# Kernel tuning notes

Measured on AMD Instinct MI355X. Metric: run time of the kernel, lower is better.

## Reference

```python
import math
import jax, jax.numpy as jnp
import numpy as np

B, Q, K, D = 16, 2048, 2048, 128

def setup_inputs() -> dict:
    key = jax.random.key(0)
    kq, kk, kv, kl = jax.random.split(key, 4)
    queries = jax.random.normal(kq, (B, Q, D), dtype=jnp.float32)
    keys = jax.random.normal(kk, (B, K, D), dtype=jnp.float32)
    values = jax.random.normal(kv, (B, K, D), dtype=jnp.float32)
    valid_lens = jax.random.randint(kl, (B,), 0, K, dtype=jnp.int64)
    return {"queries": queries, "keys": keys, "values": values, "valid_lens": valid_lens}

def reference(queries, keys, values, valid_lens):
    d = queries.shape[-1]
    # [B, Q, K] scores
    scores = jnp.einsum("bqd,bkd->bqk", queries, keys) / math.sqrt(d)
    # Original masks X[index][length:] = -1e6, i.e. along the QUERY axis (dim 1),
    # filling entire rows; softmax over the key axis then yields uniform weights
    # for those rows. Reproduce exactly.
    q_idx = jnp.arange(queries.shape[1])  # [Q]
    mask = q_idx[None, :, None] >= valid_lens[:, None, None]  # [B, Q, 1]
    scores = jnp.where(mask, jnp.float32(-1000000.0), scores)
    attention_weights = jax.nn.softmax(scores, axis=-1)
    # dropout p=0.0 (eval) -> identity
    return jnp.einsum("bqk,bkd->bqd", attention_weights, values)
```

## Files before the change

### kernel.cpp

```cpp
#include <hip/hip_runtime.h>
#include <hip/hip_bf16.h>
#include <math.h>


#define Bn 16
#define Qn 2048
#define Kn 2048
#define Dn 128
#define SCALE 0.08838834764831845f

typedef _Float16 f16;
typedef _Float16 f16x8_t __attribute__((ext_vector_type(8)));
typedef float f32x16_t __attribute__((ext_vector_type(16)));

typedef __attribute__((address_space(1))) const unsigned int glb_u32;
typedef __attribute__((address_space(3))) unsigned int lds_u32;

__device__ __forceinline__ void g2l16(const void* g, void* l) {
  __builtin_amdgcn_global_load_lds((glb_u32*)g, (lds_u32*)l, 16, 0, 0);
}


__global__ void __launch_bounds__(256) prep_kernel(
    const float* __restrict__ Kg, const float* __restrict__ Vg,
    f16* __restrict__ Kh, f16* __restrict__ Vt, float* __restrict__ sv) {
  __shared__ float ps[8][32];
  const int b = blockIdx.z;
  const int x = threadIdx.x, y = threadIdx.y;

  {
    const int lb = (b * 4 + blockIdx.y) * 32 + blockIdx.x;
    const int t = y * 32 + x;
    const size_t key = (size_t)lb * 16 + (t >> 4);
    const int G = t & 15;
    const float* kp = Kg + (key << 7) + G * 8;
    float4 f0 = *(const float4*)kp;
    float4 f1 = *(const float4*)(kp + 4);
    f16x8_t o;
    o[0] = (f16)f0.x; o[1] = (f16)f0.y; o[2] = (f16)f0.z; o[3] = (f16)f0.w;
    o[4] = (f16)f1.x; o[5] = (f16)f1.y; o[6] = (f16)f1.z; o[7] = (f16)f1.w;
    const int gs = (G & 8) | ((G & 7) ^ ((int)key & 7));
    *(f16x8_t*)(Kh + (key << 7) + (gs << 3)) = o;
  }

  const int k0 = blockIdx.x * 64, d0 = blockIdx.y * 32;
  const int d = d0 + x;
  const float* vp = Vg + ((size_t)b * Kn + k0 + y * 8) * Dn + d;
  float s = 0.f;
  f16x8_t gr;
#pragma unroll
  for (int j = 0; j < 8; j++) {
    float v = vp[(size_t)j * Dn];
    s += v;
    gr[j] = (f16)v;
  }
  {
    const int kb = k0 >> 6;
    const int G = y;
    const int gs = G ^ (d & 7);
    *(f16x8_t*)(Vt + (((size_t)(b * (Kn / 64) + kb) * 128 + d) << 6) + (gs << 3)) = gr;
  }

  ps[y][x] = s;
  __syncthreads();
  if (y == 0) {
    float tot = 0.f;
#pragma unroll
    for (int j = 0; j < 8; j++) tot += ps[j][x];
    atomicAdd(&sv[b * Dn + d0 + x], tot);
  }
}

__device__ __forceinline__ int load_vl(const int* __restrict__ vlp, int b) {
  bool is64 = true;
#pragma unroll
  for (int i = 1; i < 16; i += 2) is64 = is64 && (vlp[i] == 0);
  return is64 ? vlp[2 * b] : vlp[b];
}


template <int S>
__global__ void __launch_bounds__(256, 2) flash_kernel(
    const float* __restrict__ Qg, const f16* __restrict__ Kh,
    const f16* __restrict__ Vt, const int* __restrict__ vlp,
    f16* __restrict__ Po, float* __restrict__ Lb) {
  const int b = blockIdx.y;
  const int seg = blockIdx.z;
  const int qt = (blockIdx.x * 5 + seg * 3) & 15;
  const int q0 = qt * 128;
  const int vl = load_vl(vlp, b);
  if (q0 >= vl) return;

  __shared__ __align__(16) f16 Ks[64 * 128];
  __shared__ __align__(16) f16 Vs[128 * 64];

  const int tid = threadIdx.x;
  const int wave = tid >> 6, lane = tid & 63;
  const int H = lane >> 5, l5 = lane & 31;
  const int qbase = q0 + wave * 32;
  const bool act = qbase < vl;
  const int q_lane = qbase + l5;
  const float sc = (q_lane >= vl) ? 0.f : SCALE;

  const int krow = (l5 & 0x13) | ((l5 & 4) << 1) | ((l5 & 8) >> 1);
  const int krow7 = krow & 7;

  f16x8_t qf[8];
  if (act) {
    const float* qp = Qg + ((size_t)b * Qn + q_lane) * Dn + 8 * H;
#pragma unroll
    for (int s = 0; s < 8; s++) {
      float4 f0 = *(const float4*)(qp + 16 * s);
      float4 f1 = *(const float4*)(qp + 16 * s + 4);
      f16x8_t q8;
      q8[0] = (f16)f0.x; q8[1] = (f16)f0.y; q8[2] = (f16)f0.z; q8[3] = (f16)f0.w;
      q8[4] = (f16)f1.x; q8[5] = (f16)f1.y; q8[6] = (f16)f1.z; q8[7] = (f16)f1.w;
      qf[s] = q8;
    }
  }

  f32x16_t O[4];
#pragma unroll
  for (int i = 0; i < 4; i++) O[i] = (f32x16_t)(0.f);
  float l_lane = 0.f;

  const char* KgT = (const char*)Kh + (((size_t)b * Kn + (size_t)seg * (Kn / S)) << 8);
  const char* VgT = (const char*)Vt + ((size_t)(b * (Kn / 64) + seg * (Kn / S) / 64) << 14);

  for (int it = 0; it < (Kn / S) / 64; it++) {
    __syncthreads();
    const char* kg = KgT + (size_t)it * 16384 + wave * 4096 + lane * 16;
    const char* vg = VgT + (size_t)it * 16384 + wave * 4096 + lane * 16;
    f16* kl = Ks + wave * 2048;
    f16* vli = Vs + wave * 2048;
#pragma unroll
    for (int i = 0; i < 4; i++) {
      g2l16(kg + i * 1024, kl + i * 512);
      g2l16(vg + i * 1024, vli + i * 512);
    }
    __syncthreads();

    if (act) {
#pragma unroll
      for (int sub = 0; sub < 2; sub++) {
        f32x16_t T = (f32x16_t)(0.f);
        const f16* krp = Ks + ((sub * 32 + krow) << 7);
#pragma unroll
        for (int s = 0; s < 8; s++) {
          const int G = 2 * s + H;
          const int gs = (G & 8) | ((G & 7) ^ krow7);
          f16x8_t kf = *(const f16x8_t*)(krp + (gs << 3));
          T = __builtin_amdgcn_mfma_f32_32x32x16_f16(kf, qf[s], T, 0, 0, 0);
        }

        f16x8_t pf0, pf1;
        float ls = 0.f;
#pragma unroll
        for (int r = 0; r < 8; r++) {
          float p = __expf(T[r] * sc);
          ls += p;
          pf0[r] = (f16)p;
        }
#pragma unroll
        for (int r = 8; r < 16; r++) {
          float p = __expf(T[r] * sc);
          ls += p;
          pf1[r - 8] = (f16)p;
        }
        l_lane += ls;

#pragma unroll
        for (int dt = 0; dt < 4; dt++) {
          const f16* vrp = Vs + ((dt * 32 + l5) << 6);
          const int G0 = sub * 4 + H, G1 = sub * 4 + 2 + H;
          const int gs0 = G0 ^ (l5 & 7);
          const int gs1 = G1 ^ (l5 & 7);
          f16x8_t vf0 = *(const f16x8_t*)(vrp + (gs0 << 3));
          f16x8_t vf1 = *(const f16x8_t*)(vrp + (gs1 << 3));
          O[dt] = __builtin_amdgcn_mfma_f32_32x32x16_f16(pf0, vf0, O[dt], 0, 0, 0);
          O[dt] = __builtin_amdgcn_mfma_f32_32x32x16_f16(pf1, vf1, O[dt], 0, 0, 0);
        }
      }
    }
  }

  if (!act) return;

  l_lane += __shfl_xor(l_lane, 32);
  if (lane < 32) Lb[(size_t)(seg * Bn + b) * Qn + qbase + l5] = l_lane;

  f16* po = Po + ((size_t)(seg * Bn + b) * Qn + qbase) * Dn;
#pragma unroll
  for (int dt = 0; dt < 4; dt++) {
#pragma unroll
    for (int r = 0; r < 16; r++) {
      const int qrow = (r & 3) + 8 * (r >> 2) + 4 * H;
      po[(size_t)qrow * Dn + dt * 32 + l5] = (f16)O[dt][r];
    }
  }
}


template <int S>
__global__ void __launch_bounds__(256) combine_kernel(
    const f16* __restrict__ Po, const float* __restrict__ Lb,
    const float* __restrict__ sv, const int* __restrict__ vlp,
    float* __restrict__ Out) {
  const int b = blockIdx.y, q0 = blockIdx.x * 64;
  const int vl = load_vl(vlp, b);
  const int tid = threadIdx.x;

  __shared__ float linv[64];
  if (tid < 64) {
    float s = 0.f;
#pragma unroll
    for (int sg = 0; sg < S; sg++) s += Lb[(size_t)(sg * Bn + b) * Qn + q0 + tid];
    linv[tid] = 1.0f / s;
  }
  __syncthreads();

  const int row16 = tid >> 4;
  const int d8 = (tid & 15) * 8;
  const float invK = 1.0f / (float)Kn;
  float mv[8];
#pragma unroll
  for (int j = 0; j < 8; j++) mv[j] = sv[b * Dn + d8 + j] * invK;

#pragma unroll
  for (int pass = 0; pass < 4; pass++) {
    const int row = pass * 16 + row16;
    const int q = q0 + row;
    float acc[8];
    if (q >= vl) {
#pragma unroll
      for (int j = 0; j < 8; j++) acc[j] = mv[j];
    } else {
#pragma unroll
      for (int j = 0; j < 8; j++) acc[j] = 0.f;
#pragma unroll
      for (int sg = 0; sg < S; sg++) {
        f16x8_t v = *(const f16x8_t*)(Po + ((size_t)(sg * Bn + b) * Qn + q) * Dn + d8);
#pragma unroll
        for (int j = 0; j < 8; j++) acc[j] += (float)v[j];
      }
      const float li = linv[row];
#pragma unroll
      for (int j = 0; j < 8; j++) acc[j] *= li;
    }
    float4 o0 = make_float4(acc[0], acc[1], acc[2], acc[3]);
    float4 o1 = make_float4(acc[4], acc[5], acc[6], acc[7]);
    float* op = Out + ((size_t)b * Qn + q) * Dn + d8;
    *(float4*)op = o0;
    *(float4*)(op + 4) = o1;
  }
}


extern "C" void kernel_launch(void* const* d_in, const int* in_sizes, int n_in,
                              void* d_out, int out_size, void* d_ws, size_t ws_size,
                              hipStream_t stream) {
  const float* Qg = (const float*)d_in[0];
  const float* Kg = (const float*)d_in[1];
  const float* Vg = (const float*)d_in[2];
  const int* vl = (const int*)d_in[3];
  float* Out = (float*)d_out;

  char* ws = (char*)d_ws;
  float* sumV = (float*)ws;
  f16* Kh = (f16*)(ws + 8192);
  f16* Vt = (f16*)(ws + 8192 + (size_t)Bn * Kn * Dn * 2);
  const size_t base = 8192 + 2 * (size_t)Bn * Kn * Dn * 2;
  f16* Po = (f16*)(ws + base);

  const size_t po8 = (size_t)8 * Bn * Qn * Dn * 2;
  const size_t lb8 = (size_t)8 * Bn * Qn * 4;
  const size_t po4 = (size_t)4 * Bn * Qn * Dn * 2;
  const size_t need8 = base + po8 + lb8;

  hipMemsetAsync(sumV, 0, Bn * Dn * sizeof(float), stream);
  prep_kernel<<<dim3(32, 4, Bn), dim3(32, 8), 0, stream>>>(Kg, Vg, Kh, Vt, sumV);

  if (ws_size >= need8) {
    float* Lb = (float*)(ws + base + po8);
    flash_kernel<8><<<dim3(16, Bn, 8), 256, 0, stream>>>(Qg, Kh, Vt, vl, Po, Lb);
    combine_kernel<8><<<dim3(Qn / 64, Bn), 256, 0, stream>>>(Po, Lb, sumV, vl, Out);
  } else {
    float* Lb = (float*)(ws + base + po4);
    flash_kernel<4><<<dim3(16, Bn, 4), 256, 0, stream>>>(Qg, Kh, Vt, vl, Po, Lb);
    combine_kernel<4><<<dim3(Qn / 64, Bn), 256, 0, stream>>>(Po, Lb, sumV, vl, Out);
  }
}
```

Before: 152.7 us.

## Add KV-stationary flash kernel splitting keys into 16 segments with fp16 Q

Adds a new flash kernel that keeps a 128-key K/V tile resident in LDS and loops over query tiles, splitting the key axis into 16 segments that are merged by a 16-way combine. The prep kernel now also converts Q to fp16 and lays V out in 128-key blocks, so the flash kernel loads Q fragments directly without fp32 conversion. The aim is to load each K/V tile once per block instead of once per query tile. In exchange it needs a larger workspace for 16 partial-output planes and writes and reads more partial data in the combine step. The older sequence-split path stays as a fallback when the workspace is too small.

```diff
diff --git a/kernel.cpp b/kernel.cpp
--- a/kernel.cpp
+++ b/kernel.cpp
@@ -21,9 +21,11 @@
 }
 
 
+template <int VT>
 __global__ void __launch_bounds__(256) prep_kernel(
-    const float* __restrict__ Kg, const float* __restrict__ Vg,
-    f16* __restrict__ Kh, f16* __restrict__ Vt, float* __restrict__ sv) {
+    const float* __restrict__ Qg, const float* __restrict__ Kg,
+    const float* __restrict__ Vg, f16* __restrict__ Qh, f16* __restrict__ Kh,
+    f16* __restrict__ Vt, float* __restrict__ sv) {
   __shared__ float ps[8][32];
   const int b = blockIdx.z;
   const int x = threadIdx.x, y = threadIdx.y;
@@ -41,6 +43,15 @@
     o[4] = (f16)f1.x; o[5] = (f16)f1.y; o[6] = (f16)f1.z; o[7] = (f16)f1.w;
     const int gs = (G & 8) | ((G & 7) ^ ((int)key & 7));
     *(f16x8_t*)(Kh + (key << 7) + (gs << 3)) = o;
+    if (Qh != nullptr) {
+      const float* qp = Qg + (key << 7) + G * 8;
+      float4 q0 = *(const float4*)qp;
+      float4 q1 = *(const float4*)(qp + 4);
+      f16x8_t oq;
+      oq[0] = (f16)q0.x; oq[1] = (f16)q0.y; oq[2] = (f16)q0.z; oq[3] = (f16)q0.w;
+      oq[4] = (f16)q1.x; oq[5] = (f16)q1.y; oq[6] = (f16)q1.z; oq[7] = (f16)q1.w;
+      *(f16x8_t*)(Qh + (key << 7) + G * 8) = oq;
+    }
   }
 
   const int k0 = blockIdx.x * 64, d0 = blockIdx.y * 32;
@@ -54,7 +65,12 @@
     s += v;
     gr[j] = (f16)v;
   }
-  {
+  if (VT == 128) {
+    const int kb = k0 >> 7;
+    const int G = ((k0 & 64) >> 3) + y;
+    const int gs = (G & 8) | ((G & 7) ^ (d & 7));
+    *(f16x8_t*)(Vt + (((size_t)(b * (Kn / 128) + kb) * 128 + d) << 7) + (gs << 3)) = gr;
+  } else {
     const int kb = k0 >> 6;
     const int G = y;
     const int gs = G ^ (d & 7);
@@ -79,8 +95,121 @@
 }
 
 
+template <int J>
+__global__ void __launch_bounds__(256, 2) flash_q(
+    const f16* __restrict__ Qh, const f16* __restrict__ Kh,
+    const f16* __restrict__ Vt, const int* __restrict__ vlp,
+    f16* __restrict__ Po, float* __restrict__ Lb) {
+  const int b = blockIdx.y;
+  const int seg = blockIdx.x & 15;
+  const int j = blockIdx.x >> 4;
+  const int vl = load_vl(vlp, b);
+  const int nq = (vl + 127) >> 7;
+  if (nq == 0) return;
+
+  __shared__ __align__(16) f16 Ks[128 * 128];
+  __shared__ __align__(16) f16 Vs[128 * 128];
+
+  const int tid = threadIdx.x;
+  const int wave = tid >> 6, lane = tid & 63;
+  const int H = lane >> 5, l5 = lane & 31;
+
+  {
+    const char* kg = (const char*)Kh + (((size_t)b * Kn + seg * 128) << 8) +
+                     wave * 8192 + lane * 16;
+    const char* vg = (const char*)Vt + ((size_t)(b * (Kn / 128) + seg) << 15) +
+                     wave * 8192 + lane * 16;
+    f16* kl = Ks + wave * 4096;
+    f16* vli = Vs + wave * 4096;
+#pragma unroll
+    for (int i = 0; i < 8; i++) {
+      g2l16(kg + i * 1024, kl + i * 512);
+      g2l16(vg + i * 1024, vli + i * 512);
+    }
+  }
+  __syncthreads();
+
+  const int krow = (l5 & 0x13) | ((l5 & 4) << 1) | ((l5 & 8) >> 1);
+  const int krow7 = krow & 7;
+
+  for (int qt = j; qt < nq; qt += J) {
+    const int q0 = qt << 7;
+    const int qbase = q0 + wave * 32;
+    if (qbase >= vl) continue;
+    const int q_lane = qbase + l5;
+    const float sc = (q_lane >= vl) ? 0.f : SCALE;
+
+    f16x8_t qf[8];
+    {
+      const f16* qp = Qh + ((size_t)b * Qn + q_lane) * Dn + 8 * H;
+#pragma unroll
+      for (int s = 0; s < 8; s++) qf[s] = *(const f16x8_t*)(qp + 16 * s);
+    }
+
+    f32x16_t O[4];
+#pragma unroll
+    for (int i = 0; i < 4; i++) O[i] = (f32x16_t)(0.f);
+    float l_lane = 0.f;
+
+#pragma unroll
+    for (int sub = 0; sub < 4; sub++) {
+      f32x16_t T = (f32x16_t)(0.f);
+      const f16* krp = Ks + ((sub * 32 + krow) << 7);
+#pragma unroll
+      for (int s = 0; s < 8; s++) {
+        const int G = 2 * s + H;
+        const int gs = (G & 8) | ((G & 7) ^ krow7);
+        f16x8_t kf = *(const f16x8_t*)(krp + (gs << 3));
+        T = __builtin_amdgcn_mfma_f32_32x32x16_f16(kf, qf[s], T, 0, 0, 0);
+      }
+
+      f16x8_t pf0, pf1;
+      float ls = 0.f;
+#pragma unroll
+      for (int r = 0; r < 8; r++) {
+        float p = __expf(T[r] * sc);
+        ls += p;
+        pf0[r] = (f16)p;
+      }
+#pragma unroll
+      for (int r = 8; r < 16; r++) {
+        float p = __expf(T[r] * sc);
+        ls += p;
+        pf1[r - 8] = (f16)p;
+      }
+      l_lane += ls;
+
+#pragma unroll
+      for (int dt = 0; dt < 4; dt++) {
+        const f16* vrp = Vs + ((dt * 32 + l5) << 7);
+        const int G0 = sub * 4 + H, G1 = sub * 4 + 2 + H;
+        const int gs0 = (G0 & 8) | ((G0 & 7) ^ (l5 & 7));
+        const int gs1 = (G1 & 8) | ((G1 & 7) ^ (l5 & 7));
+        f16x8_t vf0 = *(const f16x8_t*)(vrp + (gs0 << 3));
+        f16x8_t vf1 = *(const f16x8_t*)(vrp + (gs1 << 3));
+        O[dt] = __builtin_amdgcn_mfma_f32_32x32x16_f16(pf0, vf0, O[dt], 0, 0, 0);
+        O[dt] = __builtin_amdgcn_mfma_f32_32x32x16_f16(pf1, vf1, O[dt], 0, 0, 0);
+      }
+    }
+
+    float ll = l_lane + __shfl_xor(l_lane, 32);
+    if (lane < 32) Lb[(size_t)(seg * Bn + b) * Qn + qbase + l5] = ll;
+
+    f16* po = Po + ((size_t)(seg * Bn + b) * Qn + qbase) * Dn;
+#pragma unroll
+    for (int dt = 0; dt < 4; dt++) {
+#pragma unroll
+      for (int r = 0; r < 16; r++) {
+        const int qrow = (r & 3) + 8 * (r >> 2) + 4 * H;
+        po[(size_t)qrow * Dn + dt * 32 + l5] = (f16)O[dt][r];
+      }
+    }
+  }
+}
+
+
 template <int S>
-__global__ void __launch_bounds__(256, 2) flash_kernel(
+__global__ void __launch_bounds__(256, 2) flash_seq(
     const float* __restrict__ Qg, const f16* __restrict__ Kh,
     const f16* __restrict__ Vt, const int* __restrict__ vlp,
     f16* __restrict__ Po, float* __restrict__ Lb) {
@@ -152,7 +281,6 @@
           f16x8_t kf = *(const f16x8_t*)(krp + (gs << 3));
           T = __builtin_amdgcn_mfma_f32_32x32x16_f16(kf, qf[s], T, 0, 0, 0);
         }
-
         f16x8_t pf0, pf1;
         float ls = 0.f;
 #pragma unroll
@@ -168,7 +296,6 @@
           pf1[r - 8] = (f16)p;
         }
         l_lane += ls;
-
 #pragma unroll
         for (int dt = 0; dt < 4; dt++) {
           const f16* vrp = Vs + ((dt * 32 + l5) << 6);
@@ -266,27 +393,40 @@
   float* Out = (float*)d_out;
 
   char* ws = (char*)d_ws;
+  const size_t kv = (size_t)Bn * Kn * Dn * 2;
   float* sumV = (float*)ws;
   f16* Kh = (f16*)(ws + 8192);
-  f16* Vt = (f16*)(ws + 8192 + (size_t)Bn * Kn * Dn * 2);
-  const size_t base = 8192 + 2 * (size_t)Bn * Kn * Dn * 2;
-  f16* Po = (f16*)(ws + base);
-
-  const size_t po8 = (size_t)8 * Bn * Qn * Dn * 2;
-  const size_t lb8 = (size_t)8 * Bn * Qn * 4;
-  const size_t po4 = (size_t)4 * Bn * Qn * Dn * 2;
-  const size_t need8 = base + po8 + lb8;
+  f16* Vt = (f16*)(ws + 8192 + kv);
+
+  const size_t plane = (size_t)Bn * Qn * Dn * 2;
+  const size_t lplane = (size_t)Bn * Qn * 4;
+  const size_t need16 = 8192 + 3 * kv + 16 * plane + 16 * lplane;
+  const size_t base8 = 8192 + 2 * kv;
+  const size_t need8 = base8 + 8 * plane + 8 * lplane;
 
   hipMemsetAsync(sumV, 0, Bn * Dn * sizeof(float), stream);
-  prep_kernel<<<dim3(32, 4, Bn), dim3(32, 8), 0, stream>>>(Kg, Vg, Kh, Vt, sumV);
-
-  if (ws_size >= need8) {
-    float* Lb = (float*)(ws + base + po8);
-    flash_kernel<8><<<dim3(16, Bn, 8), 256, 0, stream>>>(Qg, Kh, Vt, vl, Po, Lb);
+
+  if (ws_size >= need16) {
+    f16* Qh = (f16*)(ws + 8192 + 2 * kv);
+    f16* Po = (f16*)(ws + 8192 + 3 * kv);
+    float* Lb = (float*)(ws + 8192 + 3 * kv + 16 * plane);
+    prep_kernel<128><<<dim3(32, 4, Bn), dim3(32, 8), 0, stream>>>(
+        Qg, Kg, Vg, Qh, Kh, Vt, sumV);
+    flash_q<2><<<dim3(32, Bn), 256, 0, stream>>>(Qh, Kh, Vt, vl, Po, Lb);
+    combine_kernel<16><<<dim3(Qn / 64, Bn), 256, 0, stream>>>(Po, Lb, sumV, vl, Out);
+  } else if (ws_size >= need8) {
+    f16* Po = (f16*)(ws + base8);
+    float* Lb = (float*)(ws + base8 + 8 * plane);
+    prep_kernel<64><<<dim3(32, 4, Bn), dim3(32, 8), 0, stream>>>(
+        Qg, Kg, Vg, (f16*)nullptr, Kh, Vt, sumV);
+    flash_seq<8><<<dim3(16, Bn, 8), 256, 0, stream>>>(Qg, Kh, Vt, vl, Po, Lb);
     combine_kernel<8><<<dim3(Qn / 64, Bn), 256, 0, stream>>>(Po, Lb, sumV, vl, Out);
   } else {
-    float* Lb = (float*)(ws + base + po4);
-    flash_kernel<4><<<dim3(16, Bn, 4), 256, 0, stream>>>(Qg, Kh, Vt, vl, Po, Lb);
+    f16* Po = (f16*)(ws + base8);
+    float* Lb = (float*)(ws + base8 + 4 * plane);
+    prep_kernel<64><<<dim3(32, 4, Bn), dim3(32, 8), 0, stream>>>(
+        Qg, Kg, Vg, (f16*)nullptr, Kh, Vt, sumV);
+    flash_seq<4><<<dim3(16, Bn, 4), 256, 0, stream>>>(Qg, Kh, Vt, vl, Po, Lb);
     combine_kernel<4><<<dim3(Qn / 64, Bn), 256, 0, stream>>>(Po, Lb, sumV, vl, Out);
   }
 }
```

After: 144.3 us. -5.5%, faster.

## Fuse K/V conversion into flash kernel with key-segment-resident LDS tiles

Applied to the files above, without the earlier changes.

Removes the separate prep kernel and has each flash block load and convert a 128-key segment of K and V (with a transposed V) straight into LDS, where it stays for every query tile that block handles. The grid becomes 16 key segments times 2 query-tile groups per batch, and the combine step now reduces 16 partial outputs. This saves the f16 staging round trip through global memory and one launch, but every block reloads fp32 K/V, V is read with strided column loads, and the partial-output buffer and combine traffic grow.

```diff
diff --git a/kernel.cpp b/kernel.cpp
--- a/kernel.cpp
+++ b/kernel.cpp
@@ -13,64 +13,6 @@
 typedef _Float16 f16x8_t __attribute__((ext_vector_type(8)));
 typedef float f32x16_t __attribute__((ext_vector_type(16)));
 
-typedef __attribute__((address_space(1))) const unsigned int glb_u32;
-typedef __attribute__((address_space(3))) unsigned int lds_u32;
-
-__device__ __forceinline__ void g2l16(const void* g, void* l) {
-  __builtin_amdgcn_global_load_lds((glb_u32*)g, (lds_u32*)l, 16, 0, 0);
-}
-
-
-__global__ void __launch_bounds__(256) prep_kernel(
-    const float* __restrict__ Kg, const float* __restrict__ Vg,
-    f16* __restrict__ Kh, f16* __restrict__ Vt, float* __restrict__ sv) {
-  __shared__ float ps[8][32];
-  const int b = blockIdx.z;
-  const int x = threadIdx.x, y = threadIdx.y;
-
-  {
-    const int lb = (b * 4 + blockIdx.y) * 32 + blockIdx.x;
-    const int t = y * 32 + x;
-    const size_t key = (size_t)lb * 16 + (t >> 4);
-    const int G = t & 15;
-    const float* kp = Kg + (key << 7) + G * 8;
-    float4 f0 = *(const float4*)kp;
-    float4 f1 = *(const float4*)(kp + 4);
-    f16x8_t o;
-    o[0] = (f16)f0.x; o[1] = (f16)f0.y; o[2] = (f16)f0.z; o[3] = (f16)f0.w;
-    o[4] = (f16)f1.x; o[5] = (f16)f1.y; o[6] = (f16)f1.z; o[7] = (f16)f1.w;
-    const int gs = (G & 8) | ((G & 7) ^ ((int)key & 7));
-    *(f16x8_t*)(Kh + (key << 7) + (gs << 3)) = o;
-  }
-
-  const int k0 = blockIdx.x * 64, d0 = blockIdx.y * 32;
-  const int d = d0 + x;
-  const float* vp = Vg + ((size_t)b * Kn + k0 + y * 8) * Dn + d;
-  float s = 0.f;
-  f16x8_t gr;
-#pragma unroll
-  for (int j = 0; j < 8; j++) {
-    float v = vp[(size_t)j * Dn];
-    s += v;
-    gr[j] = (f16)v;
-  }
-  {
-    const int kb = k0 >> 6;
-    const int G = y;
-    const int gs = G ^ (d & 7);
-    *(f16x8_t*)(Vt + (((size_t)(b * (Kn / 64) + kb) * 128 + d) << 6) + (gs << 3)) = gr;
-  }
-
-  ps[y][x] = s;
-  __syncthreads();
-  if (y == 0) {
-    float tot = 0.f;
-#pragma unroll
-    for (int j = 0; j < 8; j++) tot += ps[j][x];
-    atomicAdd(&sv[b * Dn + d0 + x], tot);
-  }
-}
-
 __device__ __forceinline__ int load_vl(const int* __restrict__ vlp, int b) {
   bool is64 = true;
 #pragma unroll
@@ -79,123 +21,150 @@
 }
 
 
-template <int S>
-__global__ void __launch_bounds__(256, 2) flash_kernel(
-    const float* __restrict__ Qg, const f16* __restrict__ Kh,
-    const f16* __restrict__ Vt, const int* __restrict__ vlp,
-    f16* __restrict__ Po, float* __restrict__ Lb) {
+template <int J>
+__global__ void __launch_bounds__(256, 2) flash_g(
+    const float* __restrict__ Qg, const float* __restrict__ Kg,
+    const float* __restrict__ Vg, const int* __restrict__ vlp,
+    f16* __restrict__ Po, float* __restrict__ Lb, float* __restrict__ sv) {
   const int b = blockIdx.y;
-  const int seg = blockIdx.z;
-  const int qt = (blockIdx.x * 5 + seg * 3) & 15;
-  const int q0 = qt * 128;
+  const int seg = blockIdx.x & 15;
+  const int j = blockIdx.x >> 4;
   const int vl = load_vl(vlp, b);
-  if (q0 >= vl) return;
-
-  __shared__ __align__(16) f16 Ks[64 * 128];
-  __shared__ __align__(16) f16 Vs[128 * 64];
+  const int nq = (vl + 127) >> 7;
+  const int k0 = seg * 128;
+
+  __shared__ __align__(16) f16 Ks[128 * 128];
+  __shared__ __align__(16) f16 Vs[128 * 128];
 
   const int tid = threadIdx.x;
+
+  {
+    const int kk = tid >> 1, half = tid & 1;
+    const float* kp = Kg + ((size_t)b * Kn + k0 + kk) * Dn + half * 64;
+    f16* krow_p = Ks + kk * 128;
+    const int kk7 = kk & 7;
+#pragma unroll
+    for (int i = 0; i < 8; i++) {
+      const int G = half * 8 + i;
+      float4 f0 = *(const float4*)(kp + i * 8);
+      float4 f1 = *(const float4*)(kp + i * 8 + 4);
+      f16x8_t o;
+      o[0] = (f16)f0.x; o[1] = (f16)f0.y; o[2] = (f16)f0.z; o[3] = (f16)f0.w;
+      o[4] = (f16)f1.x; o[5] = (f16)f1.y; o[6] = (f16)f1.z; o[7] = (f16)f1.w;
+      const int gs = (G & 8) | ((G & 7) ^ kk7);
+      *(f16x8_t*)(krow_p + gs * 8) = o;
+    }
+  }
+
+  {
+    const int d = tid >> 1, half = tid & 1;
+    const float* vp = Vg + ((size_t)b * Kn + k0 + half * 64) * Dn + d;
+    f16* vrow_p = Vs + d * 128;
+    const int d7 = d & 7;
+    float colsum = 0.f;
+#pragma unroll
+    for (int i = 0; i < 8; i++) {
+      const int G = half * 8 + i;
+      f16x8_t o;
+#pragma unroll
+      for (int e = 0; e < 8; e++) {
+        float v = vp[(size_t)(i * 8 + e) * Dn];
+        o[e] = (f16)v;
+        colsum += v;
+      }
+      const int gs = (G & 8) | ((G & 7) ^ d7);
+      *(f16x8_t*)(vrow_p + gs * 8) = o;
+    }
+    if (j == 0) atomicAdd(&sv[b * Dn + d], colsum);
+  }
+  __syncthreads();
+
+  if (nq == 0) return;
+
   const int wave = tid >> 6, lane = tid & 63;
   const int H = lane >> 5, l5 = lane & 31;
-  const int qbase = q0 + wave * 32;
-  const bool act = qbase < vl;
-  const int q_lane = qbase + l5;
-  const float sc = (q_lane >= vl) ? 0.f : SCALE;
 
   const int krow = (l5 & 0x13) | ((l5 & 4) << 1) | ((l5 & 8) >> 1);
   const int krow7 = krow & 7;
 
-  f16x8_t qf[8];
-  if (act) {
-    const float* qp = Qg + ((size_t)b * Qn + q_lane) * Dn + 8 * H;
-#pragma unroll
-    for (int s = 0; s < 8; s++) {
-      float4 f0 = *(const float4*)(qp + 16 * s);
-      float4 f1 = *(const float4*)(qp + 16 * s + 4);
-      f16x8_t q8;
-      q8[0] = (f16)f0.x; q8[1] = (f16)f0.y; q8[2] = (f16)f0.z; q8[3] = (f16)f0.w;
-      q8[4] = (f16)f1.x; q8[5] = (f16)f1.y; q8[6] = (f16)f1.z; q8[7] = (f16)f1.w;
-      qf[s] = q8;
-    }
-  }
-
-  f32x16_t O[4];
-#pragma unroll
-  for (int i = 0; i < 4; i++) O[i] = (f32x16_t)(0.f);
-  float l_lane = 0.f;
-
-  const char* KgT = (const char*)Kh + (((size_t)b * Kn + (size_t)seg * (Kn / S)) << 8);
-  const char* VgT = (const char*)Vt + ((size_t)(b * (Kn / 64) + seg * (Kn / S) / 64) << 14);
-
-  for (int it = 0; it < (Kn / S) / 64; it++) {
-    __syncthreads();
-    const char* kg = KgT + (size_t)it * 16384 + wave * 4096 + lane * 16;
-    const char* vg = VgT + (size_t)it * 16384 + wave * 4096 + lane * 16;
-    f16* kl = Ks + wave * 2048;
-    f16* vli = Vs + wave * 2048;
-#pragma unroll
-    for (int i = 0; i < 4; i++) {
-      g2l16(kg + i * 1024, kl + i * 512);
-      g2l16(vg + i * 1024, vli + i * 512);
-    }
-    __syncthreads();
-
-    if (act) {
-#pragma unroll
-      for (int sub = 0; sub < 2; sub++) {
-        f32x16_t T = (f32x16_t)(0.f);
-        const f16* krp = Ks + ((sub * 32 + krow) << 7);
-#pragma unroll
-        for (int s = 0; s < 8; s++) {
-          const int G = 2 * s + H;
-          const int gs = (G & 8) | ((G & 7) ^ krow7);
-          f16x8_t kf = *(const f16x8_t*)(krp + (gs << 3));
-          T = __builtin_amdgcn_mfma_f32_32x32x16_f16(kf, qf[s], T, 0, 0, 0);
-        }
-
-        f16x8_t pf0, pf1;
-        float ls = 0.f;
-#pragma unroll
-        for (int r = 0; r < 8; r++) {
-          float p = __expf(T[r] * sc);
-          ls += p;
-          pf0[r] = (f16)p;
-        }
-#pragma unroll
-        for (int r = 8; r < 16; r++) {
-          float p = __expf(T[r] * sc);
-          ls += p;
-          pf1[r - 8] = (f16)p;
-        }
-        l_lane += ls;
-
-#pragma unroll
-        for (int dt = 0; dt < 4; dt++) {
-          const f16* vrp = Vs + ((dt * 32 + l5) << 6);
-          const int G0 = sub * 4 + H, G1 = sub * 4 + 2 + H;
-          const int gs0 = G0 ^ (l5 & 7);
-          const int gs1 = G1 ^ (l5 & 7);
-          f16x8_t vf0 = *(const f16x8_t*)(vrp + (gs0 << 3));
-          f16x8_t vf1 = *(const f16x8_t*)(vrp + (gs1 << 3));
-          O[dt] = __builtin_amdgcn_mfma_f32_32x32x16_f16(pf0, vf0, O[dt], 0, 0, 0);
-          O[dt] = __builtin_amdgcn_mfma_f32_32x32x16_f16(pf1, vf1, O[dt], 0, 0, 0);
-        }
-      }
-    }
-  }
-
-  if (!act) return;
-
-  l_lane += __shfl_xor(l_lane, 32);
-  if (lane < 32) Lb[(size_t)(seg * Bn + b) * Qn + qbase + l5] = l_lane;
-
-  f16* po = Po + ((size_t)(seg * Bn + b) * Qn + qbase) * Dn;
-#pragma unroll
-  for (int dt = 0; dt < 4; dt++) {
-#pragma unroll
-    for (int r = 0; r < 16; r++) {
-      const int qrow = (r & 3) + 8 * (r >> 2) + 4 * H;
-      po[(size_t)qrow * Dn + dt * 32 + l5] = (f16)O[dt][r];
+  for (int qt = j; qt < nq; qt += J) {
+    const int q0 = qt << 7;
+    const int qbase = q0 + wave * 32;
+    if (qbase >= vl) continue;
+    const int q_lane = qbase + l5;
+    const float sc = (q_lane >= vl) ? 0.f : SCALE;
+
+    f16x8_t qf[8];
+    {
+      const float* qp = Qg + ((size_t)b * Qn + q_lane) * Dn + 8 * H;
+#pragma unroll
+      for (int s = 0; s < 8; s++) {
+        float4 f0 = *(const float4*)(qp + 16 * s);
+        float4 f1 = *(const float4*)(qp + 16 * s + 4);
+        f16x8_t q8;
+        q8[0] = (f16)f0.x; q8[1] = (f16)f0.y; q8[2] = (f16)f0.z; q8[3] = (f16)f0.w;
+        q8[4] = (f16)f1.x; q8[5] = (f16)f1.y; q8[6] = (f16)f1.z; q8[7] = (f16)f1.w;
+        qf[s] = q8;
+      }
+    }
+
+    f32x16_t O[4];
+#pragma unroll
+    for (int i = 0; i < 4; i++) O[i] = (f32x16_t)(0.f);
+    float l_lane = 0.f;
+
+#pragma unroll
+    for (int sub = 0; sub < 4; sub++) {
+      f32x16_t T = (f32x16_t)(0.f);
+      const f16* krp = Ks + ((sub * 32 + krow) << 7);
+#pragma unroll
+      for (int s = 0; s < 8; s++) {
+        const int G = 2 * s + H;
+        const int gs = (G & 8) | ((G & 7) ^ krow7);
+        f16x8_t kf = *(const f16x8_t*)(krp + (gs << 3));
+        T = __builtin_amdgcn_mfma_f32_32x32x16_f16(kf, qf[s], T, 0, 0, 0);
+      }
+
+      f16x8_t pf0, pf1;
+      float ls = 0.f;
+#pragma unroll
+      for (int r = 0; r < 8; r++) {
+        float p = __expf(T[r] * sc);
+        ls += p;
+        pf0[r] = (f16)p;
+      }
+#pragma unroll
+      for (int r = 8; r < 16; r++) {
+        float p = __expf(T[r] * sc);
+        ls += p;
+        pf1[r - 8] = (f16)p;
+      }
+      l_lane += ls;
+
+#pragma unroll
+      for (int dt = 0; dt < 4; dt++) {
+        const f16* vrp = Vs + ((dt * 32 + l5) << 7);
+        const int G0 = sub * 4 + H, G1 = sub * 4 + 2 + H;
+        const int gs0 = (G0 & 8) | ((G0 & 7) ^ (l5 & 7));
+        const int gs1 = (G1 & 8) | ((G1 & 7) ^ (l5 & 7));
+        f16x8_t vf0 = *(const f16x8_t*)(vrp + (gs0 << 3));
+        f16x8_t vf1 = *(const f16x8_t*)(vrp + (gs1 << 3));
+        O[dt] = __builtin_amdgcn_mfma_f32_32x32x16_f16(pf0, vf0, O[dt], 0, 0, 0);
+        O[dt] = __builtin_amdgcn_mfma_f32_32x32x16_f16(pf1, vf1, O[dt], 0, 0, 0);
+      }
+    }
+
+    float ll = l_lane + __shfl_xor(l_lane, 32);
+    if (lane < 32) Lb[(size_t)(seg * Bn + b) * Qn + qbase + l5] = ll;
+
+    f16* po = Po + ((size_t)(seg * Bn + b) * Qn + qbase) * Dn;
+#pragma unroll
+    for (int dt = 0; dt < 4; dt++) {
+#pragma unroll
+      for (int r = 0; r < 16; r++) {
+        const int qrow = (r & 3) + 8 * (r >> 2) + 4 * H;
+        po[(size_t)qrow * Dn + dt * 32 + l5] = (f16)O[dt][r];
+      }
     }
   }
 }
@@ -224,7 +193,7 @@
   const float invK = 1.0f / (float)Kn;
   float mv[8];
 #pragma unroll
-  for (int j = 0; j < 8; j++) mv[j] = sv[b * Dn + d8 + j] * invK;
+  for (int jj = 0; jj < 8; jj++) mv[jj] = sv[b * Dn + d8 + jj] * invK;
 
 #pragma unroll
   for (int pass = 0; pass < 4; pass++) {
@@ -233,19 +202,19 @@
     float acc[8];
     if (q >= vl) {
 #pragma unroll
-      for (int j = 0; j < 8; j++) acc[j] = mv[j];
+      for (int jj = 0; jj < 8; jj++) acc[jj] = mv[jj];
     } else {
 #pragma unroll
-      for (int j = 0; j < 8; j++) acc[j] = 0.f;
+      for (int jj = 0; jj < 8; jj++) acc[jj] = 0.f;
 #pragma unroll
       for (int sg = 0; sg < S; sg++) {
         f16x8_t v = *(const f16x8_t*)(Po + ((size_t)(sg * Bn + b) * Qn + q) * Dn + d8);
 #pragma unroll
-        for (int j = 0; j < 8; j++) acc[j] += (float)v[j];
+        for (int jj = 0; jj < 8; jj++) acc[jj] += (float)v[jj];
       }
       const float li = linv[row];
 #pragma unroll
-      for (int j = 0; j < 8; j++) acc[j] *= li;
+      for (int jj = 0; jj < 8; jj++) acc[jj] *= li;
     }
     float4 o0 = make_float4(acc[0], acc[1], acc[2], acc[3]);
     float4 o1 = make_float4(acc[4], acc[5], acc[6], acc[7]);
@@ -266,27 +235,14 @@
   float* Out = (float*)d_out;
 
   char* ws = (char*)d_ws;
+  const size_t plane = (size_t)Bn * Qn * Dn * 2;
+  const size_t lplane = (size_t)Bn * Qn * 4;
+
   float* sumV = (float*)ws;
-  f16* Kh = (f16*)(ws + 8192);
-  f16* Vt = (f16*)(ws + 8192 + (size_t)Bn * Kn * Dn * 2);
-  const size_t base = 8192 + 2 * (size_t)Bn * Kn * Dn * 2;
-  f16* Po = (f16*)(ws + base);
-
-  const size_t po8 = (size_t)8 * Bn * Qn * Dn * 2;
-  const size_t lb8 = (size_t)8 * Bn * Qn * 4;
-  const size_t po4 = (size_t)4 * Bn * Qn * Dn * 2;
-  const size_t need8 = base + po8 + lb8;
+  f16* Po = (f16*)(ws + 8192);
+  float* Lb = (float*)(ws + 8192 + 16 * plane);
 
   hipMemsetAsync(sumV, 0, Bn * Dn * sizeof(float), stream);
-  prep_kernel<<<dim3(32, 4, Bn), dim3(32, 8), 0, stream>>>(Kg, Vg, Kh, Vt, sumV);
-
-  if (ws_size >= need8) {
-    float* Lb = (float*)(ws + base + po8);
-    flash_kernel<8><<<dim3(16, Bn, 8), 256, 0, stream>>>(Qg, Kh, Vt, vl, Po, Lb);
-    combine_kernel<8><<<dim3(Qn / 64, Bn), 256, 0, stream>>>(Po, Lb, sumV, vl, Out);
-  } else {
-    float* Lb = (float*)(ws + base + po4);
-    flash_kernel<4><<<dim3(16, Bn, 4), 256, 0, stream>>>(Qg, Kh, Vt, vl, Po, Lb);
-    combine_kernel<4><<<dim3(Qn / 64, Bn), 256, 0, stream>>>(Po, Lb, sumV, vl, Out);
-  }
-}
+  flash_g<2><<<dim3(32, Bn), 256, 0, stream>>>(Qg, Kg, Vg, vl, Po, Lb, sumV);
+  combine_kernel<16><<<dim3(Qn / 64, Bn), 256, 0, stream>>>(Po, Lb, sumV, vl, Out);
+}
```

Result: no change. 150.4 us (-1.5%).
